# Performance work log

Hardware: AMD Instinct MI355X
Metric: run time of the kernel (lower is better)

## Reference

```python
import jax, jax.numpy as jnp
import numpy as np

N_HEADS = 16
MAX_SEQ_LEN = 2048


def _rotary_tables(d_k, max_seq_len):
    # Rotary.__init__: dim//4 frequencies followed by dim//4 zeros -> dim//2 entries
    freqs = (1.0 / 10000.0) ** jnp.linspace(0.0, 1.0, d_k // 4, dtype=jnp.float32)
    freqs = jnp.concatenate([freqs, jnp.zeros(d_k // 4, dtype=jnp.float32)])
    theta = jnp.arange(max_seq_len, dtype=jnp.float32)[:, None] * freqs[None, :]  # [S, d_k//2]
    return jnp.cos(theta), jnp.sin(theta)


def _apply_rotary_bug_faithful(u, cos, sin):
    # u: [B, H, T, Dk]. Original Rotary indexes cos/sin by u.size(-3) == n_heads,
    # so the rotation angle depends on the HEAD index and broadcasts over time.
    H = u.shape[1]
    c = cos[None, :H, None, :]  # [1, H, 1, Dk//2]
    s = sin[None, :H, None, :]
    u1, u2 = jnp.split(u.astype(jnp.float32), 2, axis=-1)
    y1 = u1 * c + u2 * s
    y2 = -u1 * s + u2 * c
    return jnp.concatenate([y1, y2], axis=-1).astype(u.dtype)


def setup_inputs() -> dict:
    key = jax.random.key(0)
    k1, k2, k3 = jax.random.split(key, 3)
    d_model = 2048
    B, T = 2, 2048
    x = jax.random.normal(k1, (B, T, d_model), dtype=jnp.float32)
    w_qkv = jax.random.normal(k2, (3 * d_model, d_model), dtype=jnp.float32) * (1.0 / np.sqrt(d_model))
    w_o = jax.random.normal(k3, (d_model, d_model), dtype=jnp.float32) * (1.0 / np.sqrt(d_model))
    return {"x": x, "w_qkv": w_qkv, "w_o": w_o}


def reference(x, w_qkv, w_o):
    B, T, D = x.shape
    H = N_HEADS
    dk = D // H
    cos, sin = _rotary_tables(dk, MAX_SEQ_LEN)

    # Fused QKV projection (Linear, no bias): [B,T,3D]
    qkv = jnp.einsum('btd,ed->bte', x, w_qkv)
    qkv = qkv.reshape(B, T, 3, H, dk).transpose(2, 0, 3, 1, 4)  # [3,B,H,T,dk]
    Q, K, V = qkv[0], qkv[1], qkv[2]

    Q = _apply_rotary_bug_faithful(Q, cos, sin)
    K = _apply_rotary_bug_faithful(K, cos, sin)

    # Causal scaled dot-product attention (eval mode -> dropout_p = 0)
    scale = 1.0 / np.sqrt(dk)
    scores = jnp.einsum('bhqd,bhkd->bhqk', Q, K) * scale
    causal = jnp.tril(jnp.ones((T, T), dtype=bool))
    scores = jnp.where(causal[None, None], scores, jnp.finfo(scores.dtype).min)
    attn = jax.nn.softmax(scores, axis=-1)
    out = jnp.einsum('bhqk,bhkd->bhqd', attn, V)  # [B,H,T,dk]
    out = out.transpose(0, 2, 1, 3).reshape(B, T, D)
    return jnp.einsum('btd,ed->bte', out, w_o)
```

## Files before the change

### kernel.cpp

```cpp
#include <hip/hip_runtime.h>

typedef unsigned short u16;
typedef short bf16x8 __attribute__((ext_vector_type(8)));
typedef float f32x4 __attribute__((ext_vector_type(4)));
typedef unsigned short u16x4 __attribute__((ext_vector_type(4)));

#define QK_SCALE 0.08838834764831845f

__device__ __forceinline__ u16 f2bf(float f) {
  unsigned u = __float_as_uint(f);
  u += 0x7fffu + ((u >> 16) & 1u);
  return (u16)(u >> 16);
}
__device__ __forceinline__ float bf2f(u16 h) { return __uint_as_float(((unsigned)h) << 16); }

__device__ __forceinline__ void gld_lds16(const u16* g, u16* l) {
  __builtin_amdgcn_global_load_lds(
      (const __attribute__((address_space(1))) void*)g,
      (__attribute__((address_space(3))) void*)l, 16, 0, 0);
}

__global__ void cvt_bf16_kernel(const float* __restrict__ in, u16* __restrict__ out, int n4) {
  int i = blockIdx.x * 256 + threadIdx.x;
  if (i >= n4) return;
  const float4 v = reinterpret_cast<const float4*>(in)[i];
  u16x4 o;
  o[0] = f2bf(v.x); o[1] = f2bf(v.y); o[2] = f2bf(v.z); o[3] = f2bf(v.w);
  reinterpret_cast<u16x4*>(out)[i] = o;
}

__global__ void rotw_kernel(const float* __restrict__ w, u16* __restrict__ wb) {
  const int i = blockIdx.x * 256 + threadIdx.x;
  const int k4 = i & 511;
  const int j = (i >> 9) & 63;
  const int h = (i >> 15) & 15;
  const int which = i >> 19;
  const size_t e1 = (size_t)which * 2048 + h * 128 + j;
  const size_t e2 = e1 + 64;
  const float fr = (j < 32) ? __expf(-0.2971077539f * (float)j) : 0.0f;
  float s, c;
  __sincosf((float)h * fr, &s, &c);
  const float scale = (which == 0) ? QK_SCALE : 1.0f;
  const float4 a = reinterpret_cast<const float4*>(w + e1 * 2048)[k4];
  const float4 b = reinterpret_cast<const float4*>(w + e2 * 2048)[k4];
  u16x4 o1, o2;
  o1[0] = f2bf((a.x * c + b.x * s) * scale);
  o1[1] = f2bf((a.y * c + b.y * s) * scale);
  o1[2] = f2bf((a.z * c + b.z * s) * scale);
  o1[3] = f2bf((a.w * c + b.w * s) * scale);
  o2[0] = f2bf((b.x * c - a.x * s) * scale);
  o2[1] = f2bf((b.y * c - a.y * s) * scale);
  o2[2] = f2bf((b.z * c - a.z * s) * scale);
  o2[3] = f2bf((b.w * c - a.w * s) * scale);
  reinterpret_cast<u16x4*>(wb + e1 * 2048)[k4] = o1;
  reinterpret_cast<u16x4*>(wb + e2 * 2048)[k4] = o2;
}

template<int MODE>
__global__ __launch_bounds__(512, 2) void gemm8p_kernel(
    const u16* __restrict__ A, const u16* __restrict__ Bw, int Kdim, int n_out,
    u16* __restrict__ q_out, u16* __restrict__ k_out, u16* __restrict__ v_out,
    float* __restrict__ f_out)
{
  __shared__ __align__(16) u16 As[2][256 * 64];
  __shared__ __align__(16) u16 Bs[2][256 * 64];
  const int t = threadIdx.x, lane = t & 63, w = t >> 6;
  const int wr = w >> 2, wc = w & 3;
  const int l15 = lane & 15, lhi = lane >> 4;
  const int m0 = blockIdx.x * 256, n0 = blockIdx.y * 256;
  const int NT = Kdim >> 6;

  const int srow = w * 8 + (lane >> 3);
  const int gchunk = (lane & 7) ^ (srow & 7);
  const size_t gcol = (size_t)gchunk * 8;

  auto stageA2 = [&](int buf, int kt2, int half) {
    const size_t kb = (size_t)kt2 * 64 + gcol;
#pragma unroll
    for (int i = 0; i < 2; ++i) {
      const int ro = half * 128 + i * 64;
      gld_lds16(A + (size_t)(m0 + srow + ro) * Kdim + kb, &As[buf][(w * 8 + ro) * 64]);
    }
  };
  auto stageB4 = [&](int buf, int kt2) {
    const size_t kb = (size_t)kt2 * 64 + gcol;
#pragma unroll
    for (int ro = 0; ro < 256; ro += 64)
      gld_lds16(Bw + (size_t)(n0 + srow + ro) * Kdim + kb, &Bs[buf][(w * 8 + ro) * 64]);
  };

  const int arow0 = (wr * 128 + l15) * 64;
  const int brow0 = (wc * 64 + l15) * 64;
  const int koff0 = ((0 + lhi) ^ (l15 & 7)) * 8;
  const int koff1 = ((4 + lhi) ^ (l15 & 7)) * 8;

  f32x4 acc[8][4];
#pragma unroll
  for (int m = 0; m < 8; ++m)
#pragma unroll
    for (int n = 0; n < 4; ++n)
#pragma unroll
      for (int i = 0; i < 4; ++i) acc[m][n][i] = 0.0f;

  stageA2(0, 0, 0); stageA2(0, 0, 1);
  stageB4(0, 0);
  if (NT > 1) { stageA2(1, 1, 0); stageA2(1, 1, 1); }
  asm volatile("s_waitcnt vmcnt(4)" ::: "memory");
  __builtin_amdgcn_s_barrier();

  for (int kt = 0; kt < NT; ++kt) {
    const int cur = kt & 1;
    const u16* __restrict__ Ac = &As[cur][0];
    const u16* __restrict__ Bc = &Bs[cur][0];
    bf16x8 aK1[4], a2K1[4], b0[4], b1[4];
    {
      bf16x8 aK0[4];
#pragma unroll
      for (int m = 0; m < 4; ++m) {
        aK0[m] = *reinterpret_cast<const bf16x8*>(Ac + arow0 + m * 1024 + koff0);
        aK1[m] = *reinterpret_cast<const bf16x8*>(Ac + arow0 + m * 1024 + koff1);
      }
#pragma unroll
      for (int n = 0; n < 4; ++n)
        b0[n] = *reinterpret_cast<const bf16x8*>(Bc + brow0 + n * 1024 + koff0);
      if (kt + 1 < NT) stageB4(cur ^ 1, kt + 1);
      __builtin_amdgcn_s_barrier();
      asm volatile("s_waitcnt lgkmcnt(0)" ::: "memory");
      __builtin_amdgcn_s_setprio(1);
#pragma unroll
      for (int m = 0; m < 4; ++m)
#pragma unroll
        for (int n = 0; n < 4; ++n)
          acc[m][n] = __builtin_amdgcn_mfma_f32_16x16x32_bf16(aK0[m], b0[n], acc[m][n], 0, 0, 0);
      __builtin_amdgcn_s_setprio(0);
      __builtin_amdgcn_s_barrier();
    }
    {
      bf16x8 a2K0[4];
#pragma unroll
      for (int m = 0; m < 4; ++m) {
        a2K0[m] = *reinterpret_cast<const bf16x8*>(Ac + arow0 + (m + 4) * 1024 + koff0);
        a2K1[m] = *reinterpret_cast<const bf16x8*>(Ac + arow0 + (m + 4) * 1024 + koff1);
      }
#pragma unroll
      for (int n = 0; n < 4; ++n)
        b1[n] = *reinterpret_cast<const bf16x8*>(Bc + brow0 + n * 1024 + koff1);
      __builtin_amdgcn_s_barrier();
      asm volatile("s_waitcnt lgkmcnt(0)" ::: "memory");
      __builtin_amdgcn_s_setprio(1);
#pragma unroll
      for (int m = 0; m < 4; ++m)
#pragma unroll
        for (int n = 0; n < 4; ++n)
          acc[m + 4][n] = __builtin_amdgcn_mfma_f32_16x16x32_bf16(a2K0[m], b0[n], acc[m + 4][n], 0, 0, 0);
      __builtin_amdgcn_s_setprio(0);
      __builtin_amdgcn_s_barrier();
    }
    if (kt + 2 < NT) stageA2(cur, kt + 2, 0);
    __builtin_amdgcn_s_barrier();
    __builtin_amdgcn_s_setprio(1);
#pragma unroll
    for (int m = 0; m < 4; ++m)
#pragma unroll
      for (int n = 0; n < 4; ++n)
        acc[m][n] = __builtin_amdgcn_mfma_f32_16x16x32_bf16(aK1[m], b1[n], acc[m][n], 0, 0, 0);
    __builtin_amdgcn_s_setprio(0);
    __builtin_amdgcn_s_barrier();
    if (kt + 2 < NT) stageA2(cur, kt + 2, 1);
    __builtin_amdgcn_s_barrier();
    __builtin_amdgcn_s_setprio(1);
#pragma unroll
    for (int m = 0; m < 4; ++m)
#pragma unroll
      for (int n = 0; n < 4; ++n)
        acc[m + 4][n] = __builtin_amdgcn_mfma_f32_16x16x32_bf16(a2K1[m], b1[n], acc[m + 4][n], 0, 0, 0);
    __builtin_amdgcn_s_setprio(0);
    if (kt < NT - 2) { asm volatile("s_waitcnt vmcnt(4)" ::: "memory"); }
    else             { asm volatile("s_waitcnt vmcnt(0)" ::: "memory"); }
    __builtin_amdgcn_s_barrier();
  }

  const int rb = wr * 128 + lhi * 4;
  const int cb = wc * 64 + l15;
  if (MODE == 0) {
#pragma unroll
    for (int n = 0; n < 4; ++n) {
      const int e = n0 + cb + n * 16;
      const int which = e >> 11;
      const int h = (e >> 7) & 15;
      const int d = e & 127;
      u16* dst = (which == 0) ? q_out : (which == 1) ? k_out : v_out;
#pragma unroll
      for (int m = 0; m < 8; ++m)
#pragma unroll
        for (int r = 0; r < 4; ++r) {
          const int bt = m0 + rb + m * 16 + r;
          const int bb = bt >> 11, tt = bt & 2047;
          dst[((size_t)(bb * 16 + h) * 2048 + tt) * 128 + d] = f2bf(acc[m][n][r]);
        }
    }
  } else {
#pragma unroll
    for (int m = 0; m < 8; ++m)
#pragma unroll
      for (int r = 0; r < 4; ++r) {
        const int row = m0 + rb + m * 16 + r;
#pragma unroll
        for (int n = 0; n < 4; ++n)
          f_out[(size_t)row * n_out + n0 + cb + n * 16] = acc[m][n][r];
      }
  }
}

__global__ __launch_bounds__(256) void gemm_bt_kernel(
    const u16* __restrict__ A, const u16* __restrict__ Bw, int Kdim, int n_out,
    float* __restrict__ f_out)
{
  __shared__ __align__(16) u16 Asl[128 * 32];
  __shared__ __align__(16) u16 Bsl[128 * 32];
  const int t = threadIdx.x;
  const int lane = t & 63;
  const int w = t >> 6;
  const int wr = w >> 1, wc = w & 1;
  const int m0 = blockIdx.x * 128, n0 = blockIdx.y * 128;

  f32x4 acc[4][4];
#pragma unroll
  for (int m = 0; m < 4; ++m)
#pragma unroll
    for (int n = 0; n < 4; ++n)
#pragma unroll
      for (int i = 0; i < 4; ++i) acc[m][n][i] = 0.0f;

  const int ob0 = w * 1024 + lane * 16;
  const int row0 = ob0 >> 6;
  const int cole0 = (ob0 & 63) >> 1;
  const u16* gA0 = A + (size_t)(m0 + row0) * Kdim + cole0;
  const u16* gA1 = gA0 + (size_t)64 * Kdim;
  const u16* gB0 = Bw + (size_t)(n0 + row0) * Kdim + cole0;
  const u16* gB1 = gB0 + (size_t)64 * Kdim;
  u16* lA = Asl + w * 512;
  u16* lB = Bsl + w * 512;

  const int l15 = lane & 15;
  const int kb = (lane >> 4) * 8;

  for (int k0 = 0; k0 < Kdim; k0 += 32) {
    __syncthreads();
    gld_lds16(gA0, lA);
    gld_lds16(gA1, lA + 2048);
    gld_lds16(gB0, lB);
    gld_lds16(gB1, lB + 2048);
    gA0 += 32; gA1 += 32; gB0 += 32; gB1 += 32;
    __syncthreads();
    bf16x8 a[4], b[4];
#pragma unroll
    for (int m = 0; m < 4; ++m)
      a[m] = *reinterpret_cast<const bf16x8*>(Asl + (wr * 64 + m * 16 + l15) * 32 + kb);
#pragma unroll
    for (int n = 0; n < 4; ++n)
      b[n] = *reinterpret_cast<const bf16x8*>(Bsl + (wc * 64 + n * 16 + l15) * 32 + kb);
#pragma unroll
    for (int m = 0; m < 4; ++m)
#pragma unroll
      for (int n = 0; n < 4; ++n)
        acc[m][n] = __builtin_amdgcn_mfma_f32_16x16x32_bf16(a[m], b[n], acc[m][n], 0, 0, 0);
  }

  const int rb = wr * 64 + ((lane >> 4) << 2);
  const int cbs = wc * 64 + l15;
#pragma unroll
  for (int m = 0; m < 4; ++m)
#pragma unroll
    for (int r = 0; r < 4; ++r) {
      const int row = m0 + rb + m * 16 + r;
#pragma unroll
      for (int n = 0; n < 4; ++n)
        f_out[(size_t)row * n_out + n0 + cbs + n * 16] = acc[m][n][r];
    }
}

__global__ void transpose_v_kernel(const u16* __restrict__ V, u16* __restrict__ Vt) {
  __shared__ u16 tile[64][65];
  const int d0 = blockIdx.x * 64;
  const int t0 = blockIdx.y * 64;
  const int bh = blockIdx.z;
  const u16* src = V + (size_t)bh * (2048 * 128);
  u16* dst = Vt + (size_t)bh * (128 * 2048);
  const int tid = threadIdx.x;
  const int c4 = (tid & 15) * 4;
  const int r0 = tid >> 4;
#pragma unroll
  for (int p = 0; p < 4; ++p) {
    const int row = r0 + p * 16;
    const u16x4 v = *reinterpret_cast<const u16x4*>(src + (size_t)(t0 + row) * 128 + d0 + c4);
    tile[row][c4] = v[0]; tile[row][c4 + 1] = v[1];
    tile[row][c4 + 2] = v[2]; tile[row][c4 + 3] = v[3];
  }
  __syncthreads();
#pragma unroll
  for (int p = 0; p < 4; ++p) {
    const int dr = r0 + p * 16;
    u16x4 ov;
    ov[0] = tile[c4][dr]; ov[1] = tile[c4 + 1][dr];
    ov[2] = tile[c4 + 2][dr]; ov[3] = tile[c4 + 3][dr];
    *reinterpret_cast<u16x4*>(dst + (size_t)(d0 + dr) * 2048 + t0 + c4) = ov;
  }
}

__global__ __launch_bounds__(256) void attn_kernel(
    const u16* __restrict__ Q, const u16* __restrict__ K,
    const u16* __restrict__ Vt, u16* __restrict__ O)
{
  __shared__ __align__(16) u16 k_lds[2][64 * 128];
  __shared__ __align__(16) u16 v_lds[2][128 * 64];
  __shared__ __align__(16) u16 p_lds[4][1024];
  const int t = threadIdx.x, lane = t & 63, w = t >> 6;
  const int bh = blockIdx.y;
  const int bx = blockIdx.x;
  const int l15 = lane & 15, lhi = lane >> 4;
  const size_t qkb = (size_t)bh * (2048 * 128);
  const u16* Kg = K + qkb;
  const u16* Vg = Vt + (size_t)bh * (size_t)(128 * 2048);
  char* pw = (char*)(&p_lds[w][0]);
  const int bb = bh >> 4, h = bh & 15;
  const int kxor = (l15 & 7) << 4;

  auto stage = [&](int buf, int k0) {
#pragma unroll
    for (int ii = 0; ii < 4; ++ii) {
      const int i = w * 4 + ii;
      const int krow = i * 4 + lhi;
      gld_lds16(Kg + (size_t)(k0 + krow) * 128 + (size_t)((l15 ^ (krow & 7)) * 8),
                &k_lds[buf][i * 512]);
    }
#pragma unroll
    for (int ii = 0; ii < 4; ++ii) {
      const int i = w * 4 + ii;
      const int vrow = i * 8 + (lane >> 3);
      gld_lds16(Vg + (size_t)vrow * 2048 + k0 + (size_t)(((lane & 7) ^ (vrow & 7)) * 8),
                &v_lds[buf][i * 512]);
    }
  };

  for (int half = 0; half < 2; ++half) {
    const int qt = half ? (31 - bx) : bx;
    const int q0 = qt * 64 + w * 16;
    bf16x8 aq[4];
    {
      const u16* qp = Q + qkb + (size_t)(q0 + l15) * 128 + lhi * 8;
#pragma unroll
      for (int ks = 0; ks < 4; ++ks) aq[ks] = *reinterpret_cast<const bf16x8*>(qp + ks * 32);
    }
    f32x4 o[8];
#pragma unroll
    for (int dt = 0; dt < 8; ++dt)
#pragma unroll
      for (int i = 0; i < 4; ++i) o[dt][i] = 0.0f;
    float mrow[4] = {-1e30f, -1e30f, -1e30f, -1e30f};
    float lrow[4] = {0.f, 0.f, 0.f, 0.f};
    const int rbase = q0 + (lhi << 2);
    const int ktmax = qt;

    __syncthreads();
    stage(0, 0);
    int cur = 0;
    for (int kt = 0; kt <= ktmax; ++kt) {
      __syncthreads();
      if (kt < ktmax) stage(cur ^ 1, (kt + 1) * 64);

      const char* kbb = (const char*)(&k_lds[cur][0]);
      f32x4 s4[4];
#pragma unroll
      for (int nt = 0; nt < 4; ++nt)
#pragma unroll
        for (int i = 0; i < 4; ++i) s4[nt][i] = 0.0f;
#pragma unroll
      for (int nt = 0; nt < 4; ++nt) {
        const int krow = nt * 16 + l15;
#pragma unroll
        for (int ks = 0; ks < 4; ++ks) {
          const bf16x8 bk = *reinterpret_cast<const bf16x8*>(
              kbb + krow * 256 + ((ks * 64 + lhi * 16) ^ kxor));
          s4[nt] = __builtin_amdgcn_mfma_f32_16x16x32_bf16(aq[ks], bk, s4[nt], 0, 0, 0);
        }
      }
      if (kt == ktmax) {
#pragma unroll
        for (int nt = 0; nt < 4; ++nt) {
          const int col = kt * 64 + nt * 16 + l15;
#pragma unroll
          for (int r = 0; r < 4; ++r)
            if (col > rbase + r) s4[nt][r] = -1e30f;
        }
      }
      float alpha[4];
#pragma unroll
      for (int r = 0; r < 4; ++r) {
        float mx = fmaxf(fmaxf(s4[0][r], s4[1][r]), fmaxf(s4[2][r], s4[3][r]));
        mx = fmaxf(mx, __shfl_xor(mx, 1));
        mx = fmaxf(mx, __shfl_xor(mx, 2));
        mx = fmaxf(mx, __shfl_xor(mx, 4));
        mx = fmaxf(mx, __shfl_xor(mx, 8));
        const float mn = fmaxf(mrow[r], mx);
        alpha[r] = __expf(mrow[r] - mn);
        mrow[r] = mn;
      }
      float ps[4] = {0.f, 0.f, 0.f, 0.f};
#pragma unroll
      for (int nt = 0; nt < 4; ++nt)
#pragma unroll
        for (int r = 0; r < 4; ++r) {
          const float p = __expf(s4[nt][r] - mrow[r]);
          ps[r] += p;
          const int prow = (lhi << 2) + r;
          const int cbyte = (nt * 16 + l15) * 2;
          *(u16*)(pw + prow * 128 + (cbyte ^ ((prow & 7) << 4))) = f2bf(p);
        }
#pragma unroll
      for (int r = 0; r < 4; ++r) {
        float rs = ps[r];
        rs += __shfl_xor(rs, 1);
        rs += __shfl_xor(rs, 2);
        rs += __shfl_xor(rs, 4);
        rs += __shfl_xor(rs, 8);
        lrow[r] = lrow[r] * alpha[r] + rs;
#pragma unroll
        for (int dt = 0; dt < 8; ++dt) o[dt][r] *= alpha[r];
      }
      const char* vbb = (const char*)(&v_lds[cur][0]);
#pragma unroll
      for (int ks2 = 0; ks2 < 2; ++ks2) {
        const bf16x8 ap = *reinterpret_cast<const bf16x8*>(
            pw + l15 * 128 + ((ks2 * 64 + (lhi << 4)) ^ kxor));
#pragma unroll
        for (int dt = 0; dt < 8; ++dt) {
          const int vrow = dt * 16 + l15;
          const bf16x8 bv = *reinterpret_cast<const bf16x8*>(
              vbb + vrow * 128 + ((ks2 * 64 + lhi * 16) ^ kxor));
          o[dt] = __builtin_amdgcn_mfma_f32_16x16x32_bf16(ap, bv, o[dt], 0, 0, 0);
        }
      }
      cur ^= 1;
    }
#pragma unroll
    for (int r = 0; r < 4; ++r) {
      const float inv = 1.0f / lrow[r];
      const int row = rbase + r;
      u16* op = O + (size_t)(bb * 2048 + row) * 2048 + h * 128 + l15;
#pragma unroll
      for (int dt = 0; dt < 8; ++dt) op[dt * 16] = f2bf(o[dt][r] * inv);
    }
  }
}

extern "C" void kernel_launch(void* const* d_in, const int* in_sizes, int n_in,
                              void* d_out, int out_size, void* d_ws, size_t ws_size,
                              hipStream_t stream) {
  const float* x = (const float*)d_in[0];
  const float* wqkv = (const float*)d_in[1];
  const float* wo = (const float*)d_in[2];
  float* out = (float*)d_out;
  u16* ws = (u16*)d_ws;

  u16* xb = ws;
  u16* wqkvb = xb + 8388608;
  u16* wob = wqkvb + 12582912;
  u16* Qb = wob + 4194304;
  u16* Kb = Qb + 8388608;
  u16* Vb = Kb + 8388608;
  u16* Vtb = wqkvb;
  u16* attn = xb;

  cvt_bf16_kernel<<<8192, 256, 0, stream>>>(x, xb, 2097152);
  rotw_kernel<<<4096, 256, 0, stream>>>(wqkv, wqkvb);
  cvt_bf16_kernel<<<4096, 256, 0, stream>>>(wqkv + (size_t)4096 * 2048,
                                            wqkvb + (size_t)4096 * 2048, 1048576);
  cvt_bf16_kernel<<<4096, 256, 0, stream>>>(wo, wob, 1048576);

  gemm8p_kernel<0><<<dim3(16, 24), 512, 0, stream>>>(xb, wqkvb, 2048, 0, Qb, Kb, Vb, nullptr);

  transpose_v_kernel<<<dim3(2, 32, 32), 256, 0, stream>>>(Vb, Vtb);

  attn_kernel<<<dim3(16, 32), 256, 0, stream>>>(Qb, Kb, Vtb, attn);

  gemm_bt_kernel<<<dim3(32, 16), 256, 0, stream>>>(attn, wob, 2048, 2048, out);
}
```

Before: 311.6 us.

## Retile QKV GEMM to 128x384 blocks with K=32 stages for occupancy

```diff
diff --git a/kernel.cpp b/kernel.cpp
--- a/kernel.cpp
+++ b/kernel.cpp
@@ -56,55 +56,43 @@
   reinterpret_cast<u16x4*>(wb + e2 * 2048)[k4] = o2;
 }
 
-template<int MODE>
-__global__ __launch_bounds__(512, 2) void gemm8p_kernel(
-    const u16* __restrict__ A, const u16* __restrict__ Bw, int Kdim, int n_out,
-    u16* __restrict__ q_out, u16* __restrict__ k_out, u16* __restrict__ v_out,
-    float* __restrict__ f_out)
+__global__ __launch_bounds__(512, 4) void gemmqkv_kernel(
+    const u16* __restrict__ A, const u16* __restrict__ Bw, int Kdim,
+    u16* __restrict__ q_out, u16* __restrict__ k_out, u16* __restrict__ v_out)
 {
-  __shared__ __align__(16) u16 As[2][256 * 64];
-  __shared__ __align__(16) u16 Bs[2][256 * 64];
+  __shared__ __align__(16) u16 As[2][128 * 32];
+  __shared__ __align__(16) u16 Bs[2][384 * 32];
   const int t = threadIdx.x, lane = t & 63, w = t >> 6;
   const int wr = w >> 2, wc = w & 3;
   const int l15 = lane & 15, lhi = lane >> 4;
-  const int m0 = blockIdx.x * 256, n0 = blockIdx.y * 256;
-  const int NT = Kdim >> 6;
-
-  const int srow = w * 8 + (lane >> 3);
-  const int gchunk = (lane & 7) ^ (srow & 7);
-  const size_t gcol = (size_t)gchunk * 8;
-
-  auto stageA2 = [&](int buf, int kt2, int half) {
-    const size_t kb = (size_t)kt2 * 64 + gcol;
-#pragma unroll
-    for (int i = 0; i < 2; ++i) {
-      const int ro = half * 128 + i * 64;
-      gld_lds16(A + (size_t)(m0 + srow + ro) * Kdim + kb, &As[buf][(w * 8 + ro) * 64]);
-    }
+  const int m0 = blockIdx.x * 128, n0 = blockIdx.y * 384;
+  const int NT = Kdim >> 5;
+
+  const int srow = t >> 2;
+  const size_t gcol = (size_t)(((lane & 3) ^ ((lane >> 2) & 3)) * 8);
+
+  auto stage = [&](int buf, int kt) {
+    const size_t kb = (size_t)kt * 32 + gcol;
+    gld_lds16(A + (size_t)(m0 + srow) * Kdim + kb, &As[buf][w * 512]);
+    gld_lds16(Bw + (size_t)(n0 + srow) * Kdim + kb, &Bs[buf][w * 512]);
+    gld_lds16(Bw + (size_t)(n0 + 128 + srow) * Kdim + kb, &Bs[buf][4096 + w * 512]);
+    gld_lds16(Bw + (size_t)(n0 + 256 + srow) * Kdim + kb, &Bs[buf][8192 + w * 512]);
   };
-  auto stageB4 = [&](int buf, int kt2) {
-    const size_t kb = (size_t)kt2 * 64 + gcol;
-#pragma unroll
-    for (int ro = 0; ro < 256; ro += 64)
-      gld_lds16(Bw + (size_t)(n0 + srow + ro) * Kdim + kb, &Bs[buf][(w * 8 + ro) * 64]);
-  };
-
-  const int arow0 = (wr * 128 + l15) * 64;
-  const int brow0 = (wc * 64 + l15) * 64;
-  const int koff0 = ((0 + lhi) ^ (l15 & 7)) * 8;
-  const int koff1 = ((4 + lhi) ^ (l15 & 7)) * 8;
-
-  f32x4 acc[8][4];
-#pragma unroll
-  for (int m = 0; m < 8; ++m)
-#pragma unroll
-    for (int n = 0; n < 4; ++n)
+
+  const int arow = (wr * 64 + l15) * 32;
+  const int brow = (wc * 96 + l15) * 32;
+  const int koff = (lhi ^ (l15 & 3)) * 8;
+
+  f32x4 acc[4][6];
+#pragma unroll
+  for (int m = 0; m < 4; ++m)
+#pragma unroll
+    for (int n = 0; n < 6; ++n)
 #pragma unroll
       for (int i = 0; i < 4; ++i) acc[m][n][i] = 0.0f;
 
-  stageA2(0, 0, 0); stageA2(0, 0, 1);
-  stageB4(0, 0);
-  if (NT > 1) { stageA2(1, 1, 0); stageA2(1, 1, 1); }
+  stage(0, 0);
+  stage(1, 1);
   asm volatile("s_waitcnt vmcnt(4)" ::: "memory");
   __builtin_amdgcn_s_barrier();
 
@@ -112,102 +100,65 @@
     const int cur = kt & 1;
     const u16* __restrict__ Ac = &As[cur][0];
     const u16* __restrict__ Bc = &Bs[cur][0];
-    bf16x8 aK1[4], a2K1[4], b0[4], b1[4];
-    {
-      bf16x8 aK0[4];
-#pragma unroll
-      for (int m = 0; m < 4; ++m) {
-        aK0[m] = *reinterpret_cast<const bf16x8*>(Ac + arow0 + m * 1024 + koff0);
-        aK1[m] = *reinterpret_cast<const bf16x8*>(Ac + arow0 + m * 1024 + koff1);
-      }
-#pragma unroll
-      for (int n = 0; n < 4; ++n)
-        b0[n] = *reinterpret_cast<const bf16x8*>(Bc + brow0 + n * 1024 + koff0);
-      if (kt + 1 < NT) stageB4(cur ^ 1, kt + 1);
-      __builtin_amdgcn_s_barrier();
-      asm volatile("s_waitcnt lgkmcnt(0)" ::: "memory");
-      __builtin_amdgcn_s_setprio(1);
-#pragma unroll
-      for (int m = 0; m < 4; ++m)
-#pragma unroll
-        for (int n = 0; n < 4; ++n)
-          acc[m][n] = __builtin_amdgcn_mfma_f32_16x16x32_bf16(aK0[m], b0[n], acc[m][n], 0, 0, 0);
-      __builtin_amdgcn_s_setprio(0);
-      __builtin_amdgcn_s_barrier();
-    }
-    {
-      bf16x8 a2K0[4];
-#pragma unroll
-      for (int m = 0; m < 4; ++m) {
-        a2K0[m] = *reinterpret_cast<const bf16x8*>(Ac + arow0 + (m + 4) * 1024 + koff0);
-        a2K1[m] = *reinterpret_cast<const bf16x8*>(Ac + arow0 + (m + 4) * 1024 + koff1);
-      }
-#pragma unroll
-      for (int n = 0; n < 4; ++n)
-        b1[n] = *reinterpret_cast<const bf16x8*>(Bc + brow0 + n * 1024 + koff1);
-      __builtin_amdgcn_s_barrier();
-      asm volatile("s_waitcnt lgkmcnt(0)" ::: "memory");
-      __builtin_amdgcn_s_setprio(1);
-#pragma unroll
-      for (int m = 0; m < 4; ++m)
-#pragma unroll
-        for (int n = 0; n < 4; ++n)
-          acc[m + 4][n] = __builtin_amdgcn_mfma_f32_16x16x32_bf16(a2K0[m], b0[n], acc[m + 4][n], 0, 0, 0);
-      __builtin_amdgcn_s_setprio(0);
-      __builtin_amdgcn_s_barrier();
-    }
-    if (kt + 2 < NT) stageA2(cur, kt + 2, 0);
+    bf16x8 a[4], b[6];
+#pragma unroll
+    for (int m = 0; m < 4; ++m)
+      a[m] = *reinterpret_cast<const bf16x8*>(Ac + arow + m * 512 + koff);
+#pragma unroll
+    for (int n = 0; n < 3; ++n)
+      b[n] = *reinterpret_cast<const bf16x8*>(Bc + brow + n * 512 + koff);
     __builtin_amdgcn_s_barrier();
+    asm volatile("s_waitcnt lgkmcnt(0)" ::: "memory");
     __builtin_amdgcn_s_setprio(1);
 #pragma unroll
     for (int m = 0; m < 4; ++m)
 #pragma unroll
-      for (int n = 0; n < 4; ++n)
-        acc[m][n] = __builtin_amdgcn_mfma_f32_16x16x32_bf16(aK1[m], b1[n], acc[m][n], 0, 0, 0);
+      for (int n = 0; n < 2; ++n)
+        acc[m][n] = __builtin_amdgcn_mfma_f32_16x16x32_bf16(a[m], b[n], acc[m][n], 0, 0, 0);
     __builtin_amdgcn_s_setprio(0);
     __builtin_amdgcn_s_barrier();
-    if (kt + 2 < NT) stageA2(cur, kt + 2, 1);
+#pragma unroll
+    for (int n = 3; n < 6; ++n)
+      b[n] = *reinterpret_cast<const bf16x8*>(Bc + brow + n * 512 + koff);
     __builtin_amdgcn_s_barrier();
+    asm volatile("s_waitcnt lgkmcnt(0)" ::: "memory");
     __builtin_amdgcn_s_setprio(1);
 #pragma unroll
     for (int m = 0; m < 4; ++m)
 #pragma unroll
-      for (int n = 0; n < 4; ++n)
-        acc[m + 4][n] = __builtin_amdgcn_mfma_f32_16x16x32_bf16(a2K1[m], b1[n], acc[m + 4][n], 0, 0, 0);
+      for (int n = 2; n < 4; ++n)
+        acc[m][n] = __builtin_amdgcn_mfma_f32_16x16x32_bf16(a[m], b[n], acc[m][n], 0, 0, 0);
     __builtin_amdgcn_s_setprio(0);
-    if (kt < NT - 2) { asm volatile("s_waitcnt vmcnt(4)" ::: "memory"); }
+    __builtin_amdgcn_s_barrier();
+    if (kt + 2 < NT) stage(cur, kt + 2);
+    __builtin_amdgcn_s_setprio(1);
+#pragma unroll
+    for (int m = 0; m < 4; ++m)
+#pragma unroll
+      for (int n = 4; n < 6; ++n)
+        acc[m][n] = __builtin_amdgcn_mfma_f32_16x16x32_bf16(a[m], b[n], acc[m][n], 0, 0, 0);
+    __builtin_amdgcn_s_setprio(0);
+    if (kt + 2 < NT) { asm volatile("s_waitcnt vmcnt(4)" ::: "memory"); }
     else             { asm volatile("s_waitcnt vmcnt(0)" ::: "memory"); }
     __builtin_amdgcn_s_barrier();
   }
 
-  const int rb = wr * 128 + lhi * 4;
-  const int cb = wc * 64 + l15;
-  if (MODE == 0) {
-#pragma unroll
-    for (int n = 0; n < 4; ++n) {
-      const int e = n0 + cb + n * 16;
-      const int which = e >> 11;
-      const int h = (e >> 7) & 15;
-      const int d = e & 127;
-      u16* dst = (which == 0) ? q_out : (which == 1) ? k_out : v_out;
-#pragma unroll
-      for (int m = 0; m < 8; ++m)
-#pragma unroll
-        for (int r = 0; r < 4; ++r) {
-          const int bt = m0 + rb + m * 16 + r;
-          const int bb = bt >> 11, tt = bt & 2047;
-          dst[((size_t)(bb * 16 + h) * 2048 + tt) * 128 + d] = f2bf(acc[m][n][r]);
-        }
-    }
-  } else {
-#pragma unroll
-    for (int m = 0; m < 8; ++m)
+  const int rb = wr * 64 + lhi * 4;
+  const int cb = wc * 96 + l15;
+#pragma unroll
+  for (int n = 0; n < 6; ++n) {
+    const int e = n0 + cb + n * 16;
+    const int which = e >> 11;
+    const int h = (e >> 7) & 15;
+    const int d = e & 127;
+    u16* dst = (which == 0) ? q_out : (which == 1) ? k_out : v_out;
+#pragma unroll
+    for (int m = 0; m < 4; ++m)
 #pragma unroll
       for (int r = 0; r < 4; ++r) {
-        const int row = m0 + rb + m * 16 + r;
-#pragma unroll
-        for (int n = 0; n < 4; ++n)
-          f_out[(size_t)row * n_out + n0 + cb + n * 16] = acc[m][n][r];
+        const int bt = m0 + rb + m * 16 + r;
+        const int bb = bt >> 11, tt = bt & 2047;
+        dst[((size_t)(bb * 16 + h) * 2048 + tt) * 128 + d] = f2bf(acc[m][n][r]);
       }
   }
 }
@@ -478,7 +429,7 @@
                                             wqkvb + (size_t)4096 * 2048, 1048576);
   cvt_bf16_kernel<<<4096, 256, 0, stream>>>(wo, wob, 1048576);
 
-  gemm8p_kernel<0><<<dim3(16, 24), 512, 0, stream>>>(xb, wqkvb, 2048, 0, Qb, Kb, Vb, nullptr);
+  gemmqkv_kernel<<<dim3(32, 16), 512, 0, stream>>>(xb, wqkvb, 2048, Qb, Kb, Vb);
 
   transpose_v_kernel<<<dim3(2, 32, 32), 256, 0, stream>>>(Vb, Vtb);
 
```

Result: slower. 522.4 us (+67.6%).

## Process paired causal query tiles in one pass sharing staged K/V tiles

Applied to the files above, without the earlier changes.

```diff
diff --git a/kernel.cpp b/kernel.cpp
--- a/kernel.cpp
+++ b/kernel.cpp
@@ -318,7 +318,7 @@
   const int t = threadIdx.x, lane = t & 63, w = t >> 6;
   const int bh = blockIdx.y;
   const int bx = blockIdx.x;
-  const int l15 = lane & 15, lhi = lane >> 4;
+  const int l15 = lane & 15, lh4 = lane >> 4;
   const size_t qkb = (size_t)bh * (2048 * 128);
   const u16* Kg = K + qkb;
   const u16* Vg = Vt + (size_t)bh * (size_t)(128 * 2048);
@@ -330,7 +330,7 @@
 #pragma unroll
     for (int ii = 0; ii < 4; ++ii) {
       const int i = w * 4 + ii;
-      const int krow = i * 4 + lhi;
+      const int krow = i * 4 + lh4;
       gld_lds16(Kg + (size_t)(k0 + krow) * 128 + (size_t)((l15 ^ (krow & 7)) * 8),
                 &k_lds[buf][i * 512]);
     }
@@ -343,114 +343,105 @@
     }
   };
 
-  for (int half = 0; half < 2; ++half) {
-    const int qt = half ? (31 - bx) : bx;
-    const int q0 = qt * 64 + w * 16;
-    bf16x8 aq[4];
-    {
-      const u16* qp = Q + qkb + (size_t)(q0 + l15) * 128 + lhi * 8;
-#pragma unroll
-      for (int ks = 0; ks < 4; ++ks) aq[ks] = *reinterpret_cast<const bf16x8*>(qp + ks * 32);
-    }
-    f32x4 o[8];
-#pragma unroll
-    for (int dt = 0; dt < 8; ++dt)
-#pragma unroll
-      for (int i = 0; i < 4; ++i) o[dt][i] = 0.0f;
-    float mrow[4] = {-1e30f, -1e30f, -1e30f, -1e30f};
-    float lrow[4] = {0.f, 0.f, 0.f, 0.f};
-    const int rbase = q0 + (lhi << 2);
-    const int ktmax = qt;
-
+  const int qlo = bx, qhi = 31 - bx;
+  const int q0lo = qlo * 64 + w * 16, q0hi = qhi * 64 + w * 16;
+  const int rbLo = q0lo + (lh4 << 2), rbHi = q0hi + (lh4 << 2);
+
+  bf16x8 aqlo[4], aqhi[4];
+  {
+    const u16* qp = Q + qkb + (size_t)(q0lo + l15) * 128 + lh4 * 8;
+#pragma unroll
+    for (int ks = 0; ks < 4; ++ks) aqlo[ks] = *reinterpret_cast<const bf16x8*>(qp + ks * 32);
+  }
+  {
+    const u16* qp = Q + qkb + (size_t)(q0hi + l15) * 128 + lh4 * 8;
+#pragma unroll
+    for (int ks = 0; ks < 4; ++ks) aqhi[ks] = *reinterpret_cast<const bf16x8*>(qp + ks * 32);
+  }
+  f32x4 olo[8], ohi[8];
+#pragma unroll
+  for (int dt = 0; dt < 8; ++dt)
+#pragma unroll
+    for (int i = 0; i < 4; ++i) { olo[dt][i] = 0.0f; ohi[dt][i] = 0.0f; }
+  float mLo[4] = {-1e30f, -1e30f, -1e30f, -1e30f};
+  float lLo[4] = {0.f, 0.f, 0.f, 0.f};
+  float mHi[4] = {-1e30f, -1e30f, -1e30f, -1e30f};
+  float lHi[4] = {0.f, 0.f, 0.f, 0.f};
+
+#define TILE_BODY(AQ, OO, MM, LL, QT, RB) do { \
+    f32x4 s4[4]; \
+    _Pragma("unroll") for (int nt = 0; nt < 4; ++nt) \
+      _Pragma("unroll") for (int i = 0; i < 4; ++i) s4[nt][i] = 0.0f; \
+    _Pragma("unroll") for (int nt = 0; nt < 4; ++nt) { \
+      const int krow = nt * 16 + l15; \
+      _Pragma("unroll") for (int ks = 0; ks < 4; ++ks) { \
+        const bf16x8 bk = *reinterpret_cast<const bf16x8*>( \
+            kbb + krow * 256 + ((ks * 64 + lh4 * 16) ^ kxor)); \
+        s4[nt] = __builtin_amdgcn_mfma_f32_16x16x32_bf16(AQ[ks], bk, s4[nt], 0, 0, 0); } } \
+    if (kt == (QT)) { \
+      _Pragma("unroll") for (int nt = 0; nt < 4; ++nt) { \
+        const int col = kt * 64 + nt * 16 + l15; \
+        _Pragma("unroll") for (int r = 0; r < 4; ++r) \
+          if (col > (RB) + r) s4[nt][r] = -1e30f; } } \
+    float alpha[4]; \
+    _Pragma("unroll") for (int r = 0; r < 4; ++r) { \
+      float mx = fmaxf(fmaxf(s4[0][r], s4[1][r]), fmaxf(s4[2][r], s4[3][r])); \
+      mx = fmaxf(mx, __shfl_xor(mx, 1)); \
+      mx = fmaxf(mx, __shfl_xor(mx, 2)); \
+      mx = fmaxf(mx, __shfl_xor(mx, 4)); \
+      mx = fmaxf(mx, __shfl_xor(mx, 8)); \
+      const float mn = fmaxf(MM[r], mx); \
+      alpha[r] = __expf(MM[r] - mn); \
+      MM[r] = mn; } \
+    float ps[4] = {0.f, 0.f, 0.f, 0.f}; \
+    _Pragma("unroll") for (int nt = 0; nt < 4; ++nt) \
+      _Pragma("unroll") for (int r = 0; r < 4; ++r) { \
+        const float p = __expf(s4[nt][r] - MM[r]); \
+        ps[r] += p; \
+        const int prow = (lh4 << 2) + r; \
+        const int cbyte = (nt * 16 + l15) * 2; \
+        *(u16*)(pw + prow * 128 + (cbyte ^ ((prow & 7) << 4))) = f2bf(p); } \
+    _Pragma("unroll") for (int r = 0; r < 4; ++r) { \
+      float rs = ps[r]; \
+      rs += __shfl_xor(rs, 1); \
+      rs += __shfl_xor(rs, 2); \
+      rs += __shfl_xor(rs, 4); \
+      rs += __shfl_xor(rs, 8); \
+      LL[r] = LL[r] * alpha[r] + rs; \
+      _Pragma("unroll") for (int dt = 0; dt < 8; ++dt) OO[dt][r] *= alpha[r]; } \
+    _Pragma("unroll") for (int ks2 = 0; ks2 < 2; ++ks2) { \
+      const bf16x8 ap = *reinterpret_cast<const bf16x8*>( \
+          pw + l15 * 128 + ((ks2 * 64 + (lh4 << 4)) ^ kxor)); \
+      _Pragma("unroll") for (int dt = 0; dt < 8; ++dt) { \
+        const int vrow = dt * 16 + l15; \
+        const bf16x8 bv = *reinterpret_cast<const bf16x8*>( \
+            vbb + vrow * 128 + ((ks2 * 64 + lh4 * 16) ^ kxor)); \
+        OO[dt] = __builtin_amdgcn_mfma_f32_16x16x32_bf16(ap, bv, OO[dt], 0, 0, 0); } } \
+  } while (0)
+
+  stage(0, 0);
+  int cur = 0;
+  for (int kt = 0; kt <= qhi; ++kt) {
     __syncthreads();
-    stage(0, 0);
-    int cur = 0;
-    for (int kt = 0; kt <= ktmax; ++kt) {
-      __syncthreads();
-      if (kt < ktmax) stage(cur ^ 1, (kt + 1) * 64);
-
-      const char* kbb = (const char*)(&k_lds[cur][0]);
-      f32x4 s4[4];
-#pragma unroll
-      for (int nt = 0; nt < 4; ++nt)
-#pragma unroll
-        for (int i = 0; i < 4; ++i) s4[nt][i] = 0.0f;
-#pragma unroll
-      for (int nt = 0; nt < 4; ++nt) {
-        const int krow = nt * 16 + l15;
-#pragma unroll
-        for (int ks = 0; ks < 4; ++ks) {
-          const bf16x8 bk = *reinterpret_cast<const bf16x8*>(
-              kbb + krow * 256 + ((ks * 64 + lhi * 16) ^ kxor));
-          s4[nt] = __builtin_amdgcn_mfma_f32_16x16x32_bf16(aq[ks], bk, s4[nt], 0, 0, 0);
-        }
-      }
-      if (kt == ktmax) {
-#pragma unroll
-        for (int nt = 0; nt < 4; ++nt) {
-          const int col = kt * 64 + nt * 16 + l15;
-#pragma unroll
-          for (int r = 0; r < 4; ++r)
-            if (col > rbase + r) s4[nt][r] = -1e30f;
-        }
-      }
-      float alpha[4];
-#pragma unroll
-      for (int r = 0; r < 4; ++r) {
-        float mx = fmaxf(fmaxf(s4[0][r], s4[1][r]), fmaxf(s4[2][r], s4[3][r]));
-        mx = fmaxf(mx, __shfl_xor(mx, 1));
-        mx = fmaxf(mx, __shfl_xor(mx, 2));
-        mx = fmaxf(mx, __shfl_xor(mx, 4));
-        mx = fmaxf(mx, __shfl_xor(mx, 8));
-        const float mn = fmaxf(mrow[r], mx);
-        alpha[r] = __expf(mrow[r] - mn);
-        mrow[r] = mn;
-      }
-      float ps[4] = {0.f, 0.f, 0.f, 0.f};
-#pragma unroll
-      for (int nt = 0; nt < 4; ++nt)
-#pragma unroll
-        for (int r = 0; r < 4; ++r) {
-          const float p = __expf(s4[nt][r] - mrow[r]);
-          ps[r] += p;
-          const int prow = (lhi << 2) + r;
-          const int cbyte = (nt * 16 + l15) * 2;
-          *(u16*)(pw + prow * 128 + (cbyte ^ ((prow & 7) << 4))) = f2bf(p);
-        }
-#pragma unroll
-      for (int r = 0; r < 4; ++r) {
-        float rs = ps[r];
-        rs += __shfl_xor(rs, 1);
-        rs += __shfl_xor(rs, 2);
-        rs += __shfl_xor(rs, 4);
-        rs += __shfl_xor(rs, 8);
-        lrow[r] = lrow[r] * alpha[r] + rs;
-#pragma unroll
-        for (int dt = 0; dt < 8; ++dt) o[dt][r] *= alpha[r];
-      }
-      const char* vbb = (const char*)(&v_lds[cur][0]);
-#pragma unroll
-      for (int ks2 = 0; ks2 < 2; ++ks2) {
-        const bf16x8 ap = *reinterpret_cast<const bf16x8*>(
-            pw + l15 * 128 + ((ks2 * 64 + (lhi << 4)) ^ kxor));
-#pragma unroll
-        for (int dt = 0; dt < 8; ++dt) {
-          const int vrow = dt * 16 + l15;
-          const bf16x8 bv = *reinterpret_cast<const bf16x8*>(
-              vbb + vrow * 128 + ((ks2 * 64 + lhi * 16) ^ kxor));
-          o[dt] = __builtin_amdgcn_mfma_f32_16x16x32_bf16(ap, bv, o[dt], 0, 0, 0);
-        }
-      }
-      cur ^= 1;
-    }
-#pragma unroll
-    for (int r = 0; r < 4; ++r) {
-      const float inv = 1.0f / lrow[r];
-      const int row = rbase + r;
-      u16* op = O + (size_t)(bb * 2048 + row) * 2048 + h * 128 + l15;
-#pragma unroll
-      for (int dt = 0; dt < 8; ++dt) op[dt * 16] = f2bf(o[dt][r] * inv);
-    }
+    if (kt < qhi) stage(cur ^ 1, (kt + 1) * 64);
+    const char* kbb = (const char*)(&k_lds[cur][0]);
+    const char* vbb = (const char*)(&v_lds[cur][0]);
+    TILE_BODY(aqhi, ohi, mHi, lHi, qhi, rbHi);
+    if (kt <= qlo) TILE_BODY(aqlo, olo, mLo, lLo, qlo, rbLo);
+    cur ^= 1;
+  }
+#undef TILE_BODY
+
+#pragma unroll
+  for (int r = 0; r < 4; ++r) {
+    const float invh = 1.0f / lHi[r];
+    u16* oph = O + (size_t)(bb * 2048 + rbHi + r) * 2048 + h * 128 + l15;
+#pragma unroll
+    for (int dt = 0; dt < 8; ++dt) oph[dt * 16] = f2bf(ohi[dt][r] * invh);
+    const float invl = 1.0f / lLo[r];
+    u16* opl = O + (size_t)(bb * 2048 + rbLo + r) * 2048 + h * 128 + l15;
+#pragma unroll
+    for (int dt = 0; dt < 8; ++dt) opl[dt * 16] = f2bf(olo[dt][r] * invl);
   }
 }
 
```

Measured after the change: 363.7 us. 1.17x slower.
